# Performance work log

Measured on AMD Instinct MI355X. Metric: run time of the kernel, lower is better.

The kernel has to match this reference:

```python
import jax, jax.numpy as jnp
import numpy as np

D_MODEL = 1024
N_HEADS = 16
D_HEAD = D_MODEL // N_HEADS


def setup_inputs() -> dict:
    key = jax.random.key(0)
    ks = jax.random.split(key, 11)
    B, L = 2, 2048
    s = 1.0 / np.sqrt(D_MODEL)
    return {
        "query": jax.random.normal(ks[0], (B, L, D_MODEL), jnp.float32),
        "key": jax.random.normal(ks[1], (B, L, D_MODEL), jnp.float32),
        "value": jax.random.normal(ks[2], (B, L, D_MODEL), jnp.float32),
        "Wq": jax.random.normal(ks[3], (D_MODEL, D_MODEL), jnp.float32) * s,
        "bq": jnp.zeros((D_MODEL,), jnp.float32),
        "Wk": jax.random.normal(ks[4], (D_MODEL, D_MODEL), jnp.float32) * s,
        "bk": jnp.zeros((D_MODEL,), jnp.float32),
        "Wv": jax.random.normal(ks[5], (D_MODEL, D_MODEL), jnp.float32) * s,
        "bv": jnp.zeros((D_MODEL,), jnp.float32),
        "Wo": jax.random.normal(ks[6], (D_MODEL, D_MODEL), jnp.float32) * s,
        "bo": jnp.zeros((D_MODEL,), jnp.float32),
    }


def reference(query, key, value, Wq, bq, Wk, bk, Wv, bv, Wo, bo):
    B, Lq, _ = query.shape
    Lk = key.shape[1]
    scale = D_HEAD ** -0.5
    # projections; weights stored as [in, out] (torch Linear applies x @ W.T; here W is already transposed)
    q = (query @ Wq + bq).reshape(B, Lq, N_HEADS, D_HEAD).transpose(0, 2, 1, 3)  # [B,H,Lq,dh]
    k = (key @ Wk + bk).reshape(B, Lk, N_HEADS, D_HEAD).transpose(0, 2, 1, 3)
    v = (value @ Wv + bv).reshape(B, Lk, N_HEADS, D_HEAD).transpose(0, 2, 1, 3)
    scores = jnp.einsum('bhqd,bhkd->bhqk', q, k) * scale  # [B,H,Lq,Lk]
    # causal mask (is_causal=True)
    causal = jnp.triu(jnp.ones((Lq, Lk), dtype=bool), k=1)
    scores = jnp.where(causal, -jnp.inf, scores)
    attn = jax.nn.softmax(scores, axis=-1)
    out = jnp.einsum('bhqk,bhkd->bhqd', attn, v)  # [B,H,Lq,dh]
    out = out.transpose(0, 2, 1, 3).reshape(B, Lq, D_MODEL)
    return out @ Wo + bo
```

## Files before the change

### kernel.cpp

```cpp
#include <hip/hip_runtime.h>
#include <hip/hip_bf16.h>

typedef __bf16 bf16x8 __attribute__((ext_vector_type(8)));
typedef __bf16 bf16x4 __attribute__((ext_vector_type(4)));
typedef float floatx4 __attribute__((ext_vector_type(4)));

#define MFMA16(a, b, c) __builtin_amdgcn_mfma_f32_16x16x32_bf16(a, b, c, 0, 0, 0)
#define AS1 __attribute__((address_space(1)))
#define AS3 __attribute__((address_space(3)))

constexpr int D = 1024;
constexpr int L = 2048;
constexpr int BB = 2;
constexpr int DH = 64;
constexpr float NEG_BIG = -1e30f;
constexpr float SCALE_LOG2E = 0.125f * 1.4426950408889634f;

__device__ __forceinline__ void gld16(const __bf16* g, __bf16* l) {
  __builtin_amdgcn_global_load_lds((AS1 void*)g, (AS3 void*)l, 16, 0, 0);
}

__global__ __launch_bounds__(256) void cvt_x(const float* __restrict__ xq, const float* __restrict__ xk,
                                             const float* __restrict__ xv, __bf16* __restrict__ out) {
  const int z = blockIdx.z;
  const float* src = z == 0 ? xq : z == 1 ? xk : xv;
  __bf16* dst = out + (size_t)z * BB * L * D;
  const int N = BB * L * D;
  const int stride = gridDim.x * 256 * 4;
  for (int i = (blockIdx.x * 256 + threadIdx.x) * 4; i < N; i += stride) {
    float4 f = *(const float4*)&src[i];
    bf16x4 b = {(__bf16)f.x, (__bf16)f.y, (__bf16)f.z, (__bf16)f.w};
    *(bf16x4*)&dst[i] = b;
  }
}

__global__ void transpose_w(const float* __restrict__ w0, const float* __restrict__ w1,
                            const float* __restrict__ w2, const float* __restrict__ w3,
                            __bf16* __restrict__ out) {
  __shared__ __bf16 tile[32][33];
  int mat = blockIdx.z;
  const float* src = mat == 0 ? w0 : mat == 1 ? w1 : mat == 2 ? w2 : w3;
  __bf16* dst = out + (size_t)mat * D * D;
  int bx = blockIdx.x * 32, by = blockIdx.y * 32;
  int tx = threadIdx.x, ty = threadIdx.y;
#pragma unroll
  for (int i = 0; i < 32; i += 8)
    tile[ty + i][tx] = (__bf16)src[(size_t)(by + ty + i) * D + bx + tx];
  __syncthreads();
#pragma unroll
  for (int i = 0; i < 32; i += 8)
    dst[(size_t)(bx + ty + i) * D + by + tx] = tile[tx][ty + i];
}

__device__ __forceinline__ void stage32(const __bf16* __restrict__ A, const __bf16* __restrict__ Bt,
                                        __bf16* sA, __bf16* sB, int m0, int n0, int kb,
                                        int r, int sc, int dst) {
  gld16(&A[(size_t)(m0 + r) * 1024 + kb + sc],       &sA[dst]);
  gld16(&A[(size_t)(m0 + 64 + r) * 1024 + kb + sc],  &sA[2048 + dst]);
  gld16(&Bt[(size_t)(n0 + r) * 1024 + kb + sc],      &sB[dst]);
  gld16(&Bt[(size_t)(n0 + 64 + r) * 1024 + kb + sc], &sB[2048 + dst]);
}

__device__ __forceinline__ void gemm_core(const __bf16* __restrict__ A, const __bf16* __restrict__ Bt,
                                          __bf16* sm, int m0, int n0, int wm, int wn,
                                          int l15, int quad, int t, floatx4 (&acc)[4][4]) {
  const int r = t >> 2;
  const int sc = ((t & 3) ^ ((r >> 1) & 3)) * 8;
  const int dst = t * 8;
  const int sw2 = (l15 >> 1) & 3;

  stage32(A, Bt, sm, sm + 8192, m0, n0, 0, r, sc, dst);

  int cur = 0;
  for (int kb = 0; kb < 1024; kb += 32) {
    if (kb + 32 < 1024) {
      stage32(A, Bt, sm + (cur ^ 1) * 4096, sm + 8192 + (cur ^ 1) * 4096, m0, n0, kb + 32, r, sc, dst);
      asm volatile("s_waitcnt vmcnt(4)" ::: "memory");
    } else {
      asm volatile("s_waitcnt vmcnt(0)" ::: "memory");
    }
    __builtin_amdgcn_s_barrier();

    const __bf16* sAc = sm + cur * 4096;
    const __bf16* sBc = sm + 8192 + cur * 4096;
    bf16x8 af[4], bf_[4];
#pragma unroll
    for (int i = 0; i < 4; i++) {
      const int row = wm * 64 + i * 16 + l15;
      af[i] = *(const bf16x8*)&sAc[(row * 4 + (quad ^ sw2)) * 8];
    }
#pragma unroll
    for (int j = 0; j < 4; j++) {
      const int row = wn * 64 + j * 16 + l15;
      bf_[j] = *(const bf16x8*)&sBc[(row * 4 + (quad ^ sw2)) * 8];
    }
    asm volatile("s_waitcnt lgkmcnt(0)" ::: "memory");
    __builtin_amdgcn_sched_barrier(0);
    __builtin_amdgcn_s_barrier();

#pragma unroll
    for (int i = 0; i < 4; i++)
#pragma unroll
      for (int j = 0; j < 4; j++)
        acc[i][j] = MFMA16(af[i], bf_[j], acc[i][j]);

    cur ^= 1;
  }
}

__global__ __launch_bounds__(256, 3) void gemm_proj(const __bf16* __restrict__ xc, const __bf16* __restrict__ wt,
                                                    const float* __restrict__ bq, const float* __restrict__ bk,
                                                    const float* __restrict__ bv, __bf16* __restrict__ qkv) {
  __shared__ __align__(16) __bf16 smem[17408];

  const int flat = (blockIdx.z * 32 + blockIdx.y) * 8 + blockIdx.x;
  const int s = (flat & 7) * 96 + (flat >> 3);
  const int z = s >> 8;
  const int rem = s & 255;
  const int by = rem >> 3, bx = rem & 7;

  const __bf16* A = xc + (size_t)z * BB * L * D;
  const __bf16* Bt = wt + (size_t)z * D * D;
  const float* bias = z == 0 ? bq : z == 1 ? bk : bv;
  __bf16* dst = qkv + (size_t)z * BB * L * D;

  const int t = threadIdx.x;
  const int lane = t & 63;
  const int w = t >> 6;
  const int wm = w >> 1, wn = w & 1;
  const int l15 = lane & 15, quad = lane >> 4;
  const int m0 = by * 128, n0 = bx * 128;

  floatx4 acc[4][4];
#pragma unroll
  for (int i = 0; i < 4; i++)
#pragma unroll
    for (int j = 0; j < 4; j++) acc[i][j] = (floatx4){0.f, 0.f, 0.f, 0.f};

  gemm_core(A, Bt, smem, m0, n0, wm, wn, l15, quad, t, acc);

  float bvv[4];
#pragma unroll
  for (int j = 0; j < 4; j++) bvv[j] = bias[n0 + wn * 64 + j * 16 + l15];

  constexpr int TP = 136;
  __bf16* T = smem;
  if (z < 2) {
#pragma unroll
    for (int i = 0; i < 4; i++) {
      const int mrowb = wm * 64 + i * 16 + quad * 4;
#pragma unroll
      for (int j = 0; j < 4; j++) {
        const int ccol = wn * 64 + j * 16 + l15;
#pragma unroll
        for (int rr = 0; rr < 4; rr++) {
          float val = acc[i][j][rr] + bvv[j];
          if (z == 0) val *= SCALE_LOG2E;
          T[(mrowb + rr) * TP + ccol] = (__bf16)val;
        }
      }
    }
  } else {
#pragma unroll
    for (int i = 0; i < 4; i++) {
      const int mrowb = wm * 64 + i * 16 + quad * 4;
#pragma unroll
      for (int j = 0; j < 4; j++) {
        const int ccol = wn * 64 + j * 16 + l15;
        bf16x4 v4;
#pragma unroll
        for (int rr = 0; rr < 4; rr++) v4[rr] = (__bf16)(acc[i][j][rr] + bvv[j]);
        *(bf16x4*)&T[ccol * TP + mrowb] = v4;
      }
    }
  }
  __syncthreads();

  const int b = m0 >> 11;
  const int l0 = m0 & 2047;
  if (z < 2) {
#pragma unroll
    for (int sH = 0; sH < 8; sH++) {
      const int c = sH * 256 + t;
      const int mrow = c >> 4, k16 = c & 15;
      const int h = (n0 >> 6) + (k16 >> 3);
      const int d0 = (k16 & 7) * 8;
      bf16x8 v = *(const bf16x8*)&T[mrow * TP + k16 * 8];
      *(bf16x8*)&dst[((size_t)(b * 16 + h) * 2048 + l0 + mrow) * 64 + d0] = v;
    }
  } else {
    const int R0 = (b * 16 + (n0 >> 6)) * 64;
#pragma unroll
    for (int sH = 0; sH < 8; sH++) {
      const int c = sH * 256 + t;
      const int ccol = c >> 4, k16 = c & 15;
      bf16x8 v = *(const bf16x8*)&T[ccol * TP + k16 * 8];
      *(bf16x8*)&dst[(size_t)(R0 + ccol) * 2048 + l0 + k16 * 8] = v;
    }
  }
}

__global__ __launch_bounds__(256, 3) void gemm_o(const __bf16* __restrict__ ctx, const __bf16* __restrict__ wto,
                                                 const float* __restrict__ bo, float* __restrict__ out) {
  __shared__ __align__(16) __bf16 smem[16384];

  const int flat = blockIdx.y * 8 + blockIdx.x;
  const int s = (flat & 7) * 32 + (flat >> 3);
  const int by = s >> 3, bx = s & 7;

  const int t = threadIdx.x;
  const int lane = t & 63;
  const int w = t >> 6;
  const int wm = w >> 1, wn = w & 1;
  const int l15 = lane & 15, quad = lane >> 4;
  const int m0 = by * 128, n0 = bx * 128;

  floatx4 acc[4][4];
#pragma unroll
  for (int i = 0; i < 4; i++)
#pragma unroll
    for (int j = 0; j < 4; j++) acc[i][j] = (floatx4){0.f, 0.f, 0.f, 0.f};

  gemm_core(ctx, wto, smem, m0, n0, wm, wn, l15, quad, t, acc);

  float bvv[4];
#pragma unroll
  for (int j = 0; j < 4; j++) bvv[j] = bo[n0 + wn * 64 + j * 16 + l15];

#pragma unroll
  for (int i = 0; i < 4; i++) {
    const int rowb = m0 + wm * 64 + i * 16 + quad * 4;
#pragma unroll
    for (int j = 0; j < 4; j++) {
      const int col = n0 + wn * 64 + j * 16 + l15;
#pragma unroll
      for (int rr = 0; rr < 4; rr++)
        out[(size_t)(rowb + rr) * 1024 + col] = acc[i][j][rr] + bvv[j];
    }
  }
}

__global__ __launch_bounds__(256, 2) void flash_attn(const __bf16* __restrict__ q, const __bf16* __restrict__ k,
                                                     const __bf16* __restrict__ vT, __bf16* __restrict__ ctx) {
  __shared__ __align__(16) __bf16 kbuf[2][2][4096];
  __shared__ __align__(16) __bf16 vbuf[2][2][4096];

  const int t = threadIdx.x;
  const int lane = t & 63;
  const int w = t >> 6;
  const int l15 = lane & 15, quad = lane >> 4;
  const int bh = blockIdx.y;
  const int p = (blockIdx.x + blockIdx.y) & 15;
  const int qtA = 31 - p;
  const int qtB = p;

  const __bf16* qb = q + (size_t)bh * L * DH;
  const __bf16* kb_ = k + (size_t)bh * L * DH;
  const __bf16* vb = vT + (size_t)bh * DH * L;

  const int c0 = t, c1 = 256 + t;
  const int kr0 = c0 >> 3, kd0 = ((c0 & 7) ^ (kr0 & 7)) * 8;
  const int kr1 = c1 >> 3, kd1 = ((c1 & 7) ^ (kr1 & 7)) * 8;

  const int qrA = qtA * 64 + w * 16 + l15;
  const int qrB = qtB * 64 + w * 16 + l15;
  const bf16x8 aqA0 = *(const bf16x8*)&qb[(size_t)qrA * 64 + quad * 8];
  const bf16x8 aqA1 = *(const bf16x8*)&qb[(size_t)qrA * 64 + 32 + quad * 8];
  const bf16x8 aqB0 = *(const bf16x8*)&qb[(size_t)qrB * 64 + quad * 8];
  const bf16x8 aqB1 = *(const bf16x8*)&qb[(size_t)qrB * 64 + 32 + quad * 8];

  floatx4 oA[4], oB[4];
#pragma unroll
  for (int nt = 0; nt < 4; nt++) {
    oA[nt] = (floatx4){0.f, 0.f, 0.f, 0.f};
    oB[nt] = (floatx4){0.f, 0.f, 0.f, 0.f};
  }
  float psA = 0.f, psB = 0.f;

  auto STAGE = [&](int buf, int half, int ktile) {
    const int kt = ktile * 64;
    gld16(&kb_[(size_t)(kt + kr0) * 64 + kd0], &kbuf[buf][half][c0 * 8]);
    gld16(&kb_[(size_t)(kt + kr1) * 64 + kd1], &kbuf[buf][half][c1 * 8]);
    gld16(&vb[(size_t)kr0 * L + kt + kd0],     &vbuf[buf][half][c0 * 8]);
    gld16(&vb[(size_t)kr1 * L + kt + kd1],     &vbuf[buf][half][c1 * 8]);
  };

  auto COMPUTE = [&](int buf, int half, int ktile) {
    const int kt = ktile * 64;
    const bool diagA = (ktile == qtA);
    const bool doB   = (ktile <= qtB);
    const bool diagB = (ktile == qtB);
    const __bf16* kbh = kbuf[buf][half];
    const __bf16* vbh = vbuf[buf][half];

#pragma unroll
    for (int sp = 0; sp < 2; ++sp) {
      bf16x8 kf0[2], kf1[2];
#pragma unroll
      for (int u = 0; u < 2; ++u) {
        const int kr = (2 * sp + u) * 16 + l15;
        kf0[u] = *(const bf16x8*)&kbh[(kr * 8 + (quad ^ (kr & 7))) * 8];
        kf1[u] = *(const bf16x8*)&kbh[(kr * 8 + ((quad + 4) ^ (kr & 7))) * 8];
      }

      bf16x8 paA;
#pragma unroll
      for (int u = 0; u < 2; ++u) {
        floatx4 zz = (floatx4){0.f, 0.f, 0.f, 0.f};
        zz = MFMA16(kf0[u], aqA0, zz);
        zz = MFMA16(kf1[u], aqA1, zz);
        if (diagA) {
          const int kgb = kt + (2 * sp + u) * 16 + quad * 4;
#pragma unroll
          for (int rr = 0; rr < 4; rr++)
            if (kgb + rr > qrA) zz[rr] = NEG_BIG;
        }
#pragma unroll
        for (int rr = 0; rr < 4; rr++) {
          const float pv = __builtin_amdgcn_exp2f(zz[rr]);
          psA += pv;
          paA[u * 4 + rr] = (__bf16)pv;
        }
      }

      bf16x8 paB;
      if (doB) {
#pragma unroll
        for (int u = 0; u < 2; ++u) {
          floatx4 zz = (floatx4){0.f, 0.f, 0.f, 0.f};
          zz = MFMA16(kf0[u], aqB0, zz);
          zz = MFMA16(kf1[u], aqB1, zz);
          if (diagB) {
            const int kgb = kt + (2 * sp + u) * 16 + quad * 4;
#pragma unroll
            for (int rr = 0; rr < 4; rr++)
              if (kgb + rr > qrB) zz[rr] = NEG_BIG;
          }
#pragma unroll
          for (int rr = 0; rr < 4; rr++) {
            const float pv = __builtin_amdgcn_exp2f(zz[rr]);
            psB += pv;
            paB[u * 4 + rr] = (__bf16)pv;
          }
        }
      }

#pragma unroll
      for (int nt = 0; nt < 4; nt++) {
        const int d = nt * 16 + l15;
        const int x0 = (sp * 4 + (quad >> 1)) ^ (d & 7);
        const int x1 = (sp * 4 + 2 + (quad >> 1)) ^ (d & 7);
        union { bf16x8 v8; bf16x4 v4[2]; } uv;
        uv.v4[0] = *(const bf16x4*)&vbh[(d * 8 + x0) * 8 + (quad & 1) * 4];
        uv.v4[1] = *(const bf16x4*)&vbh[(d * 8 + x1) * 8 + (quad & 1) * 4];
        oA[nt] = MFMA16(paA, uv.v8, oA[nt]);
        if (doB) oB[nt] = MFMA16(paB, uv.v8, oB[nt]);
      }
    }
  };

  const int ntiles = qtA + 1;
  STAGE(0, 0, 0);
  STAGE(0, 1, 1);

  int it2 = 0;
#pragma unroll 1
  for (int base = 0; base < ntiles; base += 2, ++it2) {
    const int cur = it2 & 1;
    const int remn = ntiles - base - 2;

    if (remn >= 2) {
      STAGE(cur ^ 1, 0, base + 2);
      STAGE(cur ^ 1, 1, base + 3);
      asm volatile("s_waitcnt vmcnt(8)" ::: "memory");
    } else if (remn == 1) {
      STAGE(cur ^ 1, 0, base + 2);
      asm volatile("s_waitcnt vmcnt(4)" ::: "memory");
    } else {
      asm volatile("s_waitcnt vmcnt(0)" ::: "memory");
    }
    __builtin_amdgcn_s_barrier();

    COMPUTE(cur, 0, base);
    if (base + 1 < ntiles) COMPUTE(cur, 1, base + 1);

    asm volatile("s_waitcnt lgkmcnt(0)" ::: "memory");
    __builtin_amdgcn_sched_barrier(0);
    __builtin_amdgcn_s_barrier();
  }

  const int b = bh >> 4, h = bh & 15;

  psA += __shfl_xor(psA, 16);
  psA += __shfl_xor(psA, 32);
  const float invA = 1.f / psA;
#pragma unroll
  for (int rr = 0; rr < 4; rr++) {
    const float inv = __shfl(invA, (lane & 48) + quad * 4 + rr);
    const int row = qtA * 64 + w * 16 + quad * 4 + rr;
#pragma unroll
    for (int nt = 0; nt < 4; nt++) {
      const int col = h * 64 + nt * 16 + l15;
      ctx[((size_t)b * L + row) * 1024 + col] = (__bf16)(oA[nt][rr] * inv);
    }
  }

  psB += __shfl_xor(psB, 16);
  psB += __shfl_xor(psB, 32);
  const float invB = 1.f / psB;
#pragma unroll
  for (int rr = 0; rr < 4; rr++) {
    const float inv = __shfl(invB, (lane & 48) + quad * 4 + rr);
    const int row = qtB * 64 + w * 16 + quad * 4 + rr;
#pragma unroll
    for (int nt = 0; nt < 4; nt++) {
      const int col = h * 64 + nt * 16 + l15;
      ctx[((size_t)b * L + row) * 1024 + col] = (__bf16)(oB[nt][rr] * inv);
    }
  }
}

extern "C" void kernel_launch(void* const* d_in, const int* in_sizes, int n_in,
                              void* d_out, int out_size, void* d_ws, size_t ws_size,
                              hipStream_t stream) {
  const float* x_q = (const float*)d_in[0];
  const float* x_k = (const float*)d_in[1];
  const float* x_v = (const float*)d_in[2];
  const float* Wq  = (const float*)d_in[3];
  const float* bq  = (const float*)d_in[4];
  const float* Wk  = (const float*)d_in[5];
  const float* bk  = (const float*)d_in[6];
  const float* Wv  = (const float*)d_in[7];
  const float* bv  = (const float*)d_in[8];
  const float* Wo  = (const float*)d_in[9];
  const float* bo  = (const float*)d_in[10];

  char* ws = (char*)d_ws;
  __bf16* xc  = (__bf16*)ws;
  __bf16* wt  = (__bf16*)(ws + ((size_t)24 << 20));
  __bf16* qkv = (__bf16*)(ws + ((size_t)32 << 20));
  __bf16* ctx = (__bf16*)ws;
  __bf16* qp  = qkv;
  __bf16* kp  = qkv + (size_t)BB * L * D;
  __bf16* vtp = qkv + (size_t)2 * BB * L * D;

  cvt_x<<<dim3(1024, 1, 3), 256, 0, stream>>>(x_q, x_k, x_v, xc);
  transpose_w<<<dim3(32, 32, 4), dim3(32, 8), 0, stream>>>(Wq, Wk, Wv, Wo, wt);
  gemm_proj<<<dim3(8, 32, 3), 256, 0, stream>>>(xc, wt, bq, bk, bv, qkv);
  flash_attn<<<dim3(16, 32), 256, 0, stream>>>(qp, kp, vtp, ctx);
  gemm_o<<<dim3(8, 32), 256, 0, stream>>>(ctx, wt + (size_t)3 * D * D, bo, (float*)d_out);
}
```

Baseline: 206.2 us.

## Merge prep kernels and permute V^T layout for single 16-byte LDS reads

Fuses the activation conversion and weight transpose into one prep launch using a 7-deep z grid, removing a kernel launch. Separately, the projection epilogue now writes V^T with a permuted row order inside each 32-row group. The attention PV loop can then fetch each B operand with one 128-bit LDS load instead of two 64-bit loads. The permutation must line up with how the MFMA consumes the P operand along k, and both the write side and the read side change together to keep it consistent.

```diff
diff --git a/kernel.cpp b/kernel.cpp
--- a/kernel.cpp
+++ b/kernel.cpp
@@ -20,36 +20,38 @@
   __builtin_amdgcn_global_load_lds((AS1 void*)g, (AS3 void*)l, 16, 0, 0);
 }
 
-__global__ __launch_bounds__(256) void cvt_x(const float* __restrict__ xq, const float* __restrict__ xk,
-                                             const float* __restrict__ xv, __bf16* __restrict__ out) {
+__global__ __launch_bounds__(256) void prep(const float* __restrict__ xq, const float* __restrict__ xk,
+                                            const float* __restrict__ xv,
+                                            const float* __restrict__ w0, const float* __restrict__ w1,
+                                            const float* __restrict__ w2, const float* __restrict__ w3,
+                                            __bf16* __restrict__ xc, __bf16* __restrict__ wt) {
   const int z = blockIdx.z;
-  const float* src = z == 0 ? xq : z == 1 ? xk : xv;
-  __bf16* dst = out + (size_t)z * BB * L * D;
-  const int N = BB * L * D;
-  const int stride = gridDim.x * 256 * 4;
-  for (int i = (blockIdx.x * 256 + threadIdx.x) * 4; i < N; i += stride) {
-    float4 f = *(const float4*)&src[i];
-    bf16x4 b = {(__bf16)f.x, (__bf16)f.y, (__bf16)f.z, (__bf16)f.w};
-    *(bf16x4*)&dst[i] = b;
-  }
-}
-
-__global__ void transpose_w(const float* __restrict__ w0, const float* __restrict__ w1,
-                            const float* __restrict__ w2, const float* __restrict__ w3,
-                            __bf16* __restrict__ out) {
-  __shared__ __bf16 tile[32][33];
-  int mat = blockIdx.z;
-  const float* src = mat == 0 ? w0 : mat == 1 ? w1 : mat == 2 ? w2 : w3;
-  __bf16* dst = out + (size_t)mat * D * D;
-  int bx = blockIdx.x * 32, by = blockIdx.y * 32;
-  int tx = threadIdx.x, ty = threadIdx.y;
-#pragma unroll
-  for (int i = 0; i < 32; i += 8)
-    tile[ty + i][tx] = (__bf16)src[(size_t)(by + ty + i) * D + bx + tx];
-  __syncthreads();
-#pragma unroll
-  for (int i = 0; i < 32; i += 8)
-    dst[(size_t)(bx + ty + i) * D + by + tx] = tile[tx][ty + i];
+  const int t = threadIdx.x;
+  if (z < 3) {
+    const float* src = z == 0 ? xq : z == 1 ? xk : xv;
+    __bf16* dst = xc + (size_t)z * BB * L * D;
+    const int N = BB * L * D;
+    const int stride = gridDim.x * 256 * 4;
+    for (int i = (blockIdx.x * 256 + t) * 4; i < N; i += stride) {
+      float4 f = *(const float4*)&src[i];
+      bf16x4 b = {(__bf16)f.x, (__bf16)f.y, (__bf16)f.z, (__bf16)f.w};
+      *(bf16x4*)&dst[i] = b;
+    }
+  } else {
+    __shared__ __bf16 tile[32][33];
+    const int mat = z - 3;
+    const float* src = mat == 0 ? w0 : mat == 1 ? w1 : mat == 2 ? w2 : w3;
+    __bf16* dst = wt + (size_t)mat * D * D;
+    const int bx = (blockIdx.x & 31) * 32, by = (blockIdx.x >> 5) * 32;
+    const int tx = t & 31, ty = t >> 5;
+#pragma unroll
+    for (int i = 0; i < 32; i += 8)
+      tile[ty + i][tx] = (__bf16)src[(size_t)(by + ty + i) * D + bx + tx];
+    __syncthreads();
+#pragma unroll
+    for (int i = 0; i < 32; i += 8)
+      dst[(size_t)(bx + ty + i) * D + by + tx] = tile[tx][ty + i];
+  }
 }
 
 __device__ __forceinline__ void stage32(const __bf16* __restrict__ A, const __bf16* __restrict__ Bt,
@@ -163,14 +165,14 @@
   } else {
 #pragma unroll
     for (int i = 0; i < 4; i++) {
-      const int mrowb = wm * 64 + i * 16 + quad * 4;
+      const int mrowp = wm * 64 + (i >> 1) * 32 + quad * 8 + (i & 1) * 4;
 #pragma unroll
       for (int j = 0; j < 4; j++) {
         const int ccol = wn * 64 + j * 16 + l15;
         bf16x4 v4;
 #pragma unroll
         for (int rr = 0; rr < 4; rr++) v4[rr] = (__bf16)(acc[i][j][rr] + bvv[j]);
-        *(bf16x4*)&T[ccol * TP + mrowb] = v4;
+        *(bf16x4*)&T[ccol * TP + mrowp] = v4;
       }
     }
   }
@@ -348,13 +350,10 @@
 #pragma unroll
       for (int nt = 0; nt < 4; nt++) {
         const int d = nt * 16 + l15;
-        const int x0 = (sp * 4 + (quad >> 1)) ^ (d & 7);
-        const int x1 = (sp * 4 + 2 + (quad >> 1)) ^ (d & 7);
-        union { bf16x8 v8; bf16x4 v4[2]; } uv;
-        uv.v4[0] = *(const bf16x4*)&vbh[(d * 8 + x0) * 8 + (quad & 1) * 4];
-        uv.v4[1] = *(const bf16x4*)&vbh[(d * 8 + x1) * 8 + (quad & 1) * 4];
-        oA[nt] = MFMA16(paA, uv.v8, oA[nt]);
-        if (doB) oB[nt] = MFMA16(paB, uv.v8, oB[nt]);
+        const int x = (sp * 4 + quad) ^ (d & 7);
+        const bf16x8 vv = *(const bf16x8*)&vbh[(d * 8 + x) * 8];
+        oA[nt] = MFMA16(paA, vv, oA[nt]);
+        if (doB) oB[nt] = MFMA16(paB, vv, oB[nt]);
       }
     }
   };
@@ -444,8 +443,7 @@
   __bf16* kp  = qkv + (size_t)BB * L * D;
   __bf16* vtp = qkv + (size_t)2 * BB * L * D;
 
-  cvt_x<<<dim3(1024, 1, 3), 256, 0, stream>>>(x_q, x_k, x_v, xc);
-  transpose_w<<<dim3(32, 32, 4), dim3(32, 8), 0, stream>>>(Wq, Wk, Wv, Wo, wt);
+  prep<<<dim3(1024, 1, 7), 256, 0, stream>>>(x_q, x_k, x_v, Wq, Wk, Wv, Wo, xc, wt);
   gemm_proj<<<dim3(8, 32, 3), 256, 0, stream>>>(xc, wt, bq, bk, bv, qkv);
   flash_attn<<<dim3(16, 32), 256, 0, stream>>>(qp, kp, vtp, ctx);
   gemm_o<<<dim3(8, 32), 256, 0, stream>>>(ctx, wt + (size_t)3 * D * D, bo, (float*)d_out);
```

Result: no change. 203.7 us, median of 2 (-1.2%).
